# Performance work log

Measured on AMD Instinct MI355X. Metric: run time of the kernel, lower is better.

The kernel has to match this reference:

```python
import jax, jax.numpy as jnp
import numpy as np

C_CURV = 1.0   # Poincare ball curvature c
EPS = 1e-7
KERNEL = 4
STRIDE = 4


def setup_inputs() -> dict:
    key = jax.random.key(0)
    B, C, L = 16, 256, 16384
    v = jax.random.normal(key, (B, C, L), dtype=jnp.float32)
    # Project channel vectors into the Poincare ball (norm along man_dim=1 < 1)
    n = jnp.linalg.norm(v, axis=1, keepdims=True)
    x = 0.7 * v / (1.0 + n)
    return {"x": x}


def reference(x):
    # x: (B, C, L); manifold dim is axis 1 (man_dim=1)
    k, s = KERNEL, STRIDE
    B, C, L = x.shape
    out_len = (L - k) // s + 1
    # unfold along length: (out_len, k) gather indices
    idx = jnp.arange(out_len)[:, None] * s + jnp.arange(k)[None, :]
    w = x[:, :, idx]                                  # (B, C, out_len, k)
    c = C_CURV
    # Poincare -> Klein model
    x2 = jnp.sum(w * w, axis=1, keepdims=True)        # (B,1,out_len,k)
    xK = 2.0 * w / (1.0 + c * x2)
    # Lorentz factors in Klein model
    gam = 1.0 / jnp.sqrt(jnp.clip(1.0 - c * jnp.sum(xK * xK, axis=1, keepdims=True), EPS))
    # weighted Klein midpoint over the kernel window (last axis)
    mK = jnp.sum(gam * xK, axis=-1) / jnp.sum(gam, axis=-1)   # (B, C, out_len)
    # Klein -> Poincare (gyromidpoint)
    mK2 = jnp.sum(mK * mK, axis=1, keepdims=True)
    m = mK / (1.0 + jnp.sqrt(jnp.clip(1.0 - c * mK2, EPS)))
    return m
```

## Files before the change

kernel.cpp:

```cpp
#include <hip/hip_runtime.h>
#include <stdint.h>

#define B_      16
#define C_      256
#define L_      16384
#define OL_     4096
#define OT      32
#define TL      128
#define NTHR    512
#define OTILES  (OL_ / OT)

typedef float f4 __attribute__((ext_vector_type(4)));

__global__ __launch_bounds__(NTHR, 4)
void havgpool_hyp_kernel(const float* __restrict__ x, float* __restrict__ out) {
    __shared__ float sP[8][TL];
    __shared__ float sA1[TL];
    __shared__ float sQ[8][OT];
    __shared__ float sInvm[OT];

    const int t     = threadIdx.x;
    const int bid   = blockIdx.x;
    const int otile = bid & (OTILES - 1);
    const int b     = bid >> 7;
    const int j     = t & 31;
    const int rbase = t >> 5;
    const int lane  = t & 63;
    const int w     = t >> 6;

    const float* src = x + ((size_t)b * C_ * L_ + (size_t)otile * TL + 4 * j);
    f4 v[16];
    float a0 = 0.f, a1 = 0.f, a2 = 0.f, a3 = 0.f;
    #pragma unroll
    for (int it = 0; it < 16; ++it) {
        v[it] = __builtin_nontemporal_load((const f4*)(src + (size_t)(it * 16 + rbase) * L_));
        a0 += v[it].x * v[it].x;
        a1 += v[it].y * v[it].y;
        a2 += v[it].z * v[it].z;
        a3 += v[it].w * v[it].w;
    }
    a0 += __shfl_xor(a0, 32, 64);
    a1 += __shfl_xor(a1, 32, 64);
    a2 += __shfl_xor(a2, 32, 64);
    a3 += __shfl_xor(a3, 32, 64);
    if (lane < 32) {
        sP[w][4 * j + 0] = a0;
        sP[w][4 * j + 1] = a1;
        sP[w][4 * j + 2] = a2;
        sP[w][4 * j + 3] = a3;
    }
    __syncthreads();

    if (t < TL) {
        float x2 = 0.f;
        #pragma unroll
        for (int k = 0; k < 8; ++k) x2 += sP[k][t];
        const float inv1 = 1.0f / (1.0f + x2);
        const float xk2  = 4.0f * x2 * inv1 * inv1;
        const float g    = rsqrtf(fmaxf(1.0f - xk2, 1e-7f));
        float G = g;
        G += __shfl_xor(G, 1, 64);
        G += __shfl_xor(G, 2, 64);
        sA1[t] = 2.0f * g * inv1 / G;
    }
    __syncthreads();

    const float c0 = sA1[4 * j + 0];
    const float c1 = sA1[4 * j + 1];
    const float c2 = sA1[4 * j + 2];
    const float c3 = sA1[4 * j + 3];
    float mk[16];
    float q = 0.f;
    #pragma unroll
    for (int it = 0; it < 16; ++it) {
        mk[it] = v[it].x * c0 + v[it].y * c1 + v[it].z * c2 + v[it].w * c3;
        q += mk[it] * mk[it];
    }
    q += __shfl_xor(q, 32, 64);
    if (lane < 32) sQ[w][j] = q;
    __syncthreads();
    if (t < OT) {
        float m2 = 0.f;
        #pragma unroll
        for (int k = 0; k < 8; ++k) m2 += sQ[k][t];
        sInvm[t] = 1.0f / (1.0f + sqrtf(fmaxf(1.0f - m2, 1e-7f)));
    }
    __syncthreads();

    const float s = sInvm[j];
    float* op = out + (size_t)(b * C_) * OL_ + (size_t)otile * OT + j;
    #pragma unroll
    for (int it = 0; it < 16; ++it) {
        __builtin_nontemporal_store(mk[it] * s, op + (size_t)(it * 16 + rbase) * OL_);
    }
}

extern "C" void kernel_launch(void* const* d_in, const int* in_sizes, int n_in,
                              void* d_out, int out_size, void* d_ws, size_t ws_size,
                              hipStream_t stream) {
    const float* x = (const float*)d_in[0];
    float* out = (float*)d_out;
    havgpool_hyp_kernel<<<dim3(OTILES * B_), NTHR, 0, stream>>>(x, out);
}
```

Measured before the change: 349.9 us.

## Process four tiles per block with register prefetch of the next tile

```diff
diff --git a/kernel.cpp b/kernel.cpp
--- a/kernel.cpp
+++ b/kernel.cpp
@@ -8,9 +8,16 @@
 #define OT      32
 #define TL      128
 #define NTHR    512
-#define OTILES  (OL_ / OT)
+#define TPB     4
+#define NBLK    ((B_ * (OL_ / OT)) / TPB)
 
 typedef float f4 __attribute__((ext_vector_type(4)));
+
+#define BARRIER_LGKM() do {                                   \
+    asm volatile("s_waitcnt lgkmcnt(0)" ::: "memory");        \
+    __builtin_amdgcn_s_barrier();                             \
+    asm volatile("" ::: "memory");                            \
+} while (0)
 
 __global__ __launch_bounds__(NTHR, 4)
 void havgpool_hyp_kernel(const float* __restrict__ x, float* __restrict__ out) {
@@ -20,78 +27,93 @@
     __shared__ float sInvm[OT];
 
     const int t     = threadIdx.x;
-    const int bid   = blockIdx.x;
-    const int otile = bid & (OTILES - 1);
-    const int b     = bid >> 7;
+    const int blk   = blockIdx.x;
+    const int tile0 = blk * TPB;
+    const int b     = tile0 >> 7;
+    const int ot0   = tile0 & 127;
     const int j     = t & 31;
     const int rbase = t >> 5;
     const int lane  = t & 63;
     const int w     = t >> 6;
 
-    const float* src = x + ((size_t)b * C_ * L_ + (size_t)otile * TL + 4 * j);
+    const float* src = x   + ((size_t)b * C_ * L_  + (size_t)ot0 * TL + 4 * j);
+    float*       op  = out + ((size_t)b * C_ * OL_ + (size_t)ot0 * OT + j);
+
     f4 v[16];
-    float a0 = 0.f, a1 = 0.f, a2 = 0.f, a3 = 0.f;
     #pragma unroll
-    for (int it = 0; it < 16; ++it) {
+    for (int it = 0; it < 16; ++it)
         v[it] = __builtin_nontemporal_load((const f4*)(src + (size_t)(it * 16 + rbase) * L_));
-        a0 += v[it].x * v[it].x;
-        a1 += v[it].y * v[it].y;
-        a2 += v[it].z * v[it].z;
-        a3 += v[it].w * v[it].w;
-    }
-    a0 += __shfl_xor(a0, 32, 64);
-    a1 += __shfl_xor(a1, 32, 64);
-    a2 += __shfl_xor(a2, 32, 64);
-    a3 += __shfl_xor(a3, 32, 64);
-    if (lane < 32) {
-        sP[w][4 * j + 0] = a0;
-        sP[w][4 * j + 1] = a1;
-        sP[w][4 * j + 2] = a2;
-        sP[w][4 * j + 3] = a3;
-    }
-    __syncthreads();
 
-    if (t < TL) {
-        float x2 = 0.f;
+    #pragma unroll
+    for (int i = 0; i < TPB; ++i) {
+        const float* nsrc = src + (size_t)(i + 1) * TL;
+
+        float a0 = 0.f, a1 = 0.f, a2 = 0.f, a3 = 0.f;
         #pragma unroll
-        for (int k = 0; k < 8; ++k) x2 += sP[k][t];
-        const float inv1 = 1.0f / (1.0f + x2);
-        const float xk2  = 4.0f * x2 * inv1 * inv1;
-        const float g    = rsqrtf(fmaxf(1.0f - xk2, 1e-7f));
-        float G = g;
-        G += __shfl_xor(G, 1, 64);
-        G += __shfl_xor(G, 2, 64);
-        sA1[t] = 2.0f * g * inv1 / G;
-    }
-    __syncthreads();
+        for (int it = 0; it < 16; ++it) {
+            a0 += v[it].x * v[it].x;
+            a1 += v[it].y * v[it].y;
+            a2 += v[it].z * v[it].z;
+            a3 += v[it].w * v[it].w;
+        }
+        a0 += __shfl_xor(a0, 32, 64);
+        a1 += __shfl_xor(a1, 32, 64);
+        a2 += __shfl_xor(a2, 32, 64);
+        a3 += __shfl_xor(a3, 32, 64);
+        if (lane < 32) {
+            sP[w][4 * j + 0] = a0;
+            sP[w][4 * j + 1] = a1;
+            sP[w][4 * j + 2] = a2;
+            sP[w][4 * j + 3] = a3;
+        }
+        BARRIER_LGKM();
 
-    const float c0 = sA1[4 * j + 0];
-    const float c1 = sA1[4 * j + 1];
-    const float c2 = sA1[4 * j + 2];
-    const float c3 = sA1[4 * j + 3];
-    float mk[16];
-    float q = 0.f;
-    #pragma unroll
-    for (int it = 0; it < 16; ++it) {
-        mk[it] = v[it].x * c0 + v[it].y * c1 + v[it].z * c2 + v[it].w * c3;
-        q += mk[it] * mk[it];
-    }
-    q += __shfl_xor(q, 32, 64);
-    if (lane < 32) sQ[w][j] = q;
-    __syncthreads();
-    if (t < OT) {
-        float m2 = 0.f;
+        if (t < TL) {
+            float x2 = 0.f;
+            #pragma unroll
+            for (int k = 0; k < 8; ++k) x2 += sP[k][t];
+            const float inv1 = 1.0f / (1.0f + x2);
+            const float xk2  = 4.0f * x2 * inv1 * inv1;
+            const float g    = rsqrtf(fmaxf(1.0f - xk2, 1e-7f));
+            float G = g;
+            G += __shfl_xor(G, 1, 64);
+            G += __shfl_xor(G, 2, 64);
+            sA1[t] = 2.0f * g * inv1 / G;
+        }
+        BARRIER_LGKM();
+
+        const float c0 = sA1[4 * j + 0];
+        const float c1 = sA1[4 * j + 1];
+        const float c2 = sA1[4 * j + 2];
+        const float c3 = sA1[4 * j + 3];
+        float mk[16];
+        float q = 0.f;
         #pragma unroll
-        for (int k = 0; k < 8; ++k) m2 += sQ[k][t];
-        sInvm[t] = 1.0f / (1.0f + sqrtf(fmaxf(1.0f - m2, 1e-7f)));
-    }
-    __syncthreads();
+        for (int it = 0; it < 16; ++it) {
+            const f4 vv = v[it];
+            const float m = vv.x * c0 + vv.y * c1 + vv.z * c2 + vv.w * c3;
+            mk[it] = m;
+            q += m * m;
+            if (i < TPB - 1)
+                v[it] = __builtin_nontemporal_load((const f4*)(nsrc + (size_t)(it * 16 + rbase) * L_));
+        }
+        q += __shfl_xor(q, 32, 64);
+        if (lane < 32) sQ[w][j] = q;
+        BARRIER_LGKM();
 
-    const float s = sInvm[j];
-    float* op = out + (size_t)(b * C_) * OL_ + (size_t)otile * OT + j;
-    #pragma unroll
-    for (int it = 0; it < 16; ++it) {
-        __builtin_nontemporal_store(mk[it] * s, op + (size_t)(it * 16 + rbase) * OL_);
+        if (t < OT) {
+            float m2 = 0.f;
+            #pragma unroll
+            for (int k = 0; k < 8; ++k) m2 += sQ[k][t];
+            sInvm[t] = 1.0f / (1.0f + sqrtf(fmaxf(1.0f - m2, 1e-7f)));
+        }
+        BARRIER_LGKM();
+
+        const float s = sInvm[j];
+        #pragma unroll
+        for (int it = 0; it < 16; ++it)
+            __builtin_nontemporal_store(mk[it] * s,
+                op + (size_t)(it * 16 + rbase) * OL_ + (size_t)i * OT);
     }
 }
 
@@ -100,5 +122,5 @@
                               hipStream_t stream) {
     const float* x = (const float*)d_in[0];
     float* out = (float*)d_out;
-    havgpool_hyp_kernel<<<dim3(OTILES * B_), NTHR, 0, stream>>>(x, out);
+    havgpool_hyp_kernel<<<dim3(NBLK), NTHR, 0, stream>>>(x, out);
 }
```

Result: slower. 361.1 us (+3.2%).
